# Kernel tuning notes

Measured on AMD Instinct MI355X. Metric: run time of the kernel, lower is better.

## Reference

```python
import jax, jax.numpy as jnp
import numpy as np

# Dims from LiftSplatShootGPN defaults
B, N, D, FH, FW, C = 8, 6, 41, 8, 22, 64
OGFH, OGFW = 128, 352
DX = jnp.array([0.5, 0.5, 20.0], dtype=jnp.float32)        # gen_dx_bx
BX = jnp.array([-49.75, -49.75, 0.0], dtype=jnp.float32)
NX = (200, 200, 1)


def _frustum():
    # D x fH x fW x 3, matches create_frustum
    ds = jnp.broadcast_to(jnp.arange(4.0, 45.0, 1.0, dtype=jnp.float32).reshape(D, 1, 1), (D, FH, FW))
    xs = jnp.broadcast_to(jnp.linspace(0.0, OGFW - 1.0, FW, dtype=jnp.float32).reshape(1, 1, FW), (D, FH, FW))
    ys = jnp.broadcast_to(jnp.linspace(0.0, OGFH - 1.0, FH, dtype=jnp.float32).reshape(1, FH, 1), (D, FH, FW))
    return jnp.stack((xs, ys, ds), -1)


def setup_inputs() -> dict:
    key = jax.random.key(0)
    k1, k2, k3, k4, k5, k6 = jax.random.split(key, 6)
    eye = jnp.eye(3, dtype=jnp.float32)
    x_feats = jax.random.normal(k1, (B, N, D, FH, FW, C), dtype=jnp.float32)
    # well-conditioned camera extrinsics / intrinsics
    rots = eye + 0.1 * jax.random.normal(k2, (B, N, 3, 3), dtype=jnp.float32)
    trans = 2.0 * jax.random.normal(k3, (B, N, 3), dtype=jnp.float32)
    intr_base = jnp.array([[278.0, 0.0, 176.0], [0.0, 278.0, 64.0], [0.0, 0.0, 1.0]], dtype=jnp.float32)
    intrins = intr_base + 0.5 * jax.random.normal(k4, (B, N, 3, 3), dtype=jnp.float32) * jnp.array([[1, 0, 1], [0, 1, 1], [0, 0, 0]], dtype=jnp.float32)
    post_rots = eye + 0.01 * jax.random.normal(k5, (B, N, 3, 3), dtype=jnp.float32)
    post_trans = 0.5 * jax.random.normal(k6, (B, N, 3), dtype=jnp.float32)
    return {"x_feats": x_feats, "rots": rots, "trans": trans, "intrins": intrins,
            "post_rots": post_rots, "post_trans": post_trans}


def _forward(x_feats, rots, trans, intrins, post_rots, post_trans):
    frustum = _frustum()  # [D,FH,FW,3]
    # get_geometry: undo image-space augmentation
    pts = frustum[None, None] - post_trans[:, :, None, None, None, :]            # [B,N,D,H,W,3]
    inv_pr = jnp.linalg.inv(post_rots)                                           # [B,N,3,3]
    pts = jnp.einsum('bnij,bndhwj->bndhwi', inv_pr, pts)
    # unproject: (u*d, v*d, d)
    pts = jnp.concatenate((pts[..., :2] * pts[..., 2:3], pts[..., 2:3]), axis=-1)
    combine = jnp.einsum('bnij,bnjk->bnik', rots, jnp.linalg.inv(intrins))
    geom = jnp.einsum('bnij,bndhwj->bndhwi', combine, pts) + trans[:, :, None, None, None, :]

    # voxel_pooling
    Nprime = B * N * D * FH * FW
    x = x_feats.reshape(Nprime, C)
    # torch .long() truncates toward zero -> astype(int32) matches
    g = ((geom - (BX - DX / 2.0)) / DX).reshape(Nprime, 3).astype(jnp.int32)
    bix = jnp.repeat(jnp.arange(B, dtype=jnp.int32), Nprime // B)
    kept = ((g[:, 0] >= 0) & (g[:, 0] < NX[0]) &
            (g[:, 1] >= 0) & (g[:, 1] < NX[1]) &
            (g[:, 2] >= 0) & (g[:, 2] < NX[2]))
    # QuickCumsum computes per-voxel segment sums; scatter-add of all kept points
    # into the dense grid yields identical values without the sort.
    flat = ((bix * NX[2] + g[:, 2]) * NX[0] + g[:, 0]) * NX[1] + g[:, 1]
    flat = jnp.where(kept, flat, 0)
    xm = jnp.where(kept[:, None], x, jnp.zeros((), x.dtype))
    grid = jnp.zeros((B * NX[2] * NX[0] * NX[1], C), dtype=x.dtype).at[flat].add(xm)
    # final: [B, C, nz, nx0, nx1] -> cat over nz (nz=1) -> [B, C, 200, 200]
    grid = grid.reshape(B, NX[2], NX[0], NX[1], C)
    final = jnp.transpose(grid, (0, 1, 4, 2, 3)).reshape(B, NX[2] * C, NX[0], NX[1])
    return final


def reference(x_feats, rots, trans, intrins, post_rots, post_trans):
    return _forward(x_feats, rots, trans, intrins, post_rots, post_trans)
```

## Files before the change

### kernel.cpp

```cpp
#include <hip/hip_runtime.h>

#define B_   8
#define N_   6
#define D_   41
#define FH_  8
#define FW_  22
#define C_   64
#define NPRIME (B_*N_*D_*FH_*FW_)
#define NBLK_PTS 1353
#define NX0  200
#define NX1  200
#define G1Q  4
#define NB2  (B_ * NX0 * G1Q)
#define OUTSZ (B_*C_*NX0*NX1)
#define CAP  128
#define DIRECT_N 16
#define MAXTASKS 16384
#define GATHER_BLOCKS 1024

__device__ void lapack_inv3_f32(const float Ain[9], float Aout[9]) {
    #pragma clang fp contract(off)
    float a[9];
    for (int r = 0; r < 3; ++r)
        for (int c = 0; c < 3; ++c)
            a[c*3 + r] = Ain[r*3 + c];
    int ipiv[3];
    for (int j = 0; j < 3; ++j) {
        int p = j;
        float amax = fabsf(a[j*3 + j]);
        for (int i = j + 1; i < 3; ++i) {
            float v = fabsf(a[j*3 + i]);
            if (v > amax) { amax = v; p = i; }
        }
        ipiv[j] = p;
        if (p != j)
            for (int c = 0; c < 3; ++c) { float t = a[c*3+j]; a[c*3+j] = a[c*3+p]; a[c*3+p] = t; }
        float d = 1.0f / a[j*3 + j];
        for (int i = j + 1; i < 3; ++i) a[j*3 + i] = a[j*3 + i] * d;
        for (int jj = j + 1; jj < 3; ++jj) {
            float temp = -a[jj*3 + j];
            for (int ii = j + 1; ii < 3; ++ii)
                a[jj*3 + ii] = a[jj*3 + ii] + a[j*3 + ii] * temp;
        }
    }
    for (int j = 0; j < 3; ++j) {
        float ajj_inv = 1.0f / a[j*3 + j];
        a[j*3 + j] = ajj_inv;
        float AJJ = -ajj_inv;
        for (int jj = 0; jj < j; ++jj) {
            float temp = a[j*3 + jj];
            for (int i = 0; i < jj; ++i)
                a[j*3 + i] = a[j*3 + i] + temp * a[jj*3 + i];
            a[j*3 + jj] = a[j*3 + jj] * a[jj*3 + jj];
        }
        for (int i = 0; i < j; ++i) a[j*3 + i] = a[j*3 + i] * AJJ;
    }
    float work[3];
    for (int j = 2; j >= 0; --j) {
        for (int i = j + 1; i < 3; ++i) { work[i] = a[j*3 + i]; a[j*3 + i] = 0.0f; }
        for (int jj = j + 1; jj < 3; ++jj) {
            float temp = -work[jj];
            for (int i = 0; i < 3; ++i)
                a[j*3 + i] = a[j*3 + i] + temp * a[jj*3 + i];
        }
    }
    for (int j = 2; j >= 0; --j) {
        int p = ipiv[j];
        if (p != j)
            for (int i = 0; i < 3; ++i) { float t = a[j*3+i]; a[j*3+i] = a[p*3+i]; a[p*3+i] = t; }
    }
    for (int r = 0; r < 3; ++r)
        for (int c = 0; c < 3; ++c)
            Aout[r*3 + c] = a[c*3 + r];
}

__global__ void prep_kernel(const float* __restrict__ rots,
                            const float* __restrict__ trans,
                            const float* __restrict__ intrins,
                            const float* __restrict__ post_rots,
                            const float* __restrict__ post_trans,
                            float* __restrict__ mats,
                            int* __restrict__ counts) {
    #pragma clang fp contract(off)
    int t = threadIdx.x;
    for (int i = t; i < NB2; i += 256) counts[i] = 0;
    if (t >= B_ * N_) return;
    float pr[9], ipr[9], K[9], iK[9];
    for (int i = 0; i < 9; ++i) { pr[i] = post_rots[t*9 + i]; K[i] = intrins[t*9 + i]; }
    lapack_inv3_f32(pr, ipr);
    lapack_inv3_f32(K, iK);
    float* m = mats + t * 24;
    for (int i = 0; i < 9; ++i) m[i] = ipr[i];
    for (int i = 0; i < 3; ++i)
        for (int k = 0; k < 3; ++k) {
            float s = rots[t*9 + i*3 + 0] * iK[0*3 + k];
            s = s + rots[t*9 + i*3 + 1] * iK[1*3 + k];
            s = s + rots[t*9 + i*3 + 2] * iK[2*3 + k];
            m[9 + i*3 + k] = s;
        }
    for (int i = 0; i < 3; ++i) {
        m[18 + i] = post_trans[t*3 + i];
        m[21 + i] = trans[t*3 + i];
    }
}

__global__ void __launch_bounds__(256) geom_kernel(
        const float* __restrict__ mats,
        unsigned int* __restrict__ pcode,
        int* __restrict__ counts,
        float4* __restrict__ out4) {
    #pragma clang fp contract(off)
    __shared__ unsigned int hist[NB2];
    int t = threadIdx.x;
    int p = blockIdx.x * 256 + t;
    for (int i = t; i < NB2; i += 256) hist[i] = 0u;
    __syncthreads();

    int w  = p % FW_;
    int h  = (p / FW_) % FH_;
    int d  = (p / (FW_ * FH_)) % D_;
    int bn = p / (FW_ * FH_ * D_);
    int b  = bn / N_;

    const float* m = mats + bn * 24;

    float xs = (w == FW_ - 1) ? 351.0f : (float)((double)w * (351.0 / 21.0));
    float ys = (h == FH_ - 1) ? 127.0f : (float)((double)h * (127.0 / 7.0));
    float ds = 4.0f + (float)d;

    float px = xs - m[18], py = ys - m[19], pz = ds - m[20];
    float qx = m[0]*px;  qx = qx + m[1]*py;  qx = qx + m[2]*pz;
    float qy = m[3]*px;  qy = qy + m[4]*py;  qy = qy + m[5]*pz;
    float qz = m[6]*px;  qz = qz + m[7]*py;  qz = qz + m[8]*pz;

    float ux = qx * qz, uy = qy * qz, uz = qz;

    float gx = m[9]*ux;   gx = gx + m[10]*uy;  gx = gx + m[11]*uz;  gx = gx + m[21];
    float gy = m[12]*ux;  gy = gy + m[13]*uy;  gy = gy + m[14]*uz;  gy = gy + m[22];
    float gz = m[15]*ux;  gz = gz + m[16]*uy;  gz = gz + m[17]*uz;  gz = gz + m[23];

    float cx = (gx - (-50.0f)) / 0.5f;
    float cy = (gy - (-50.0f)) / 0.5f;
    float cz = (gz - (-10.0f)) / 20.0f;
    int g0 = (int)cx;
    int g1 = (int)cy;
    int g2 = (int)cz;

    bool kept = (g0 >= 0) && (g0 < NX0) && (g1 >= 0) && (g1 < NX1) && (g2 == 0);
    if (kept) {
        int g1q = g1 / 50;
        int g1r = g1 - g1q * 50;
        int bk  = (b * NX0 + g0) * G1Q + g1q;
        pcode[p] = ((unsigned int)bk << 6) | (unsigned int)g1r;
        atomicAdd(&hist[bk], 1u);
    } else {
        pcode[p] = 0xFFFFFFFFu;
    }
    __syncthreads();
    for (int i = t; i < NB2; i += 256) {
        unsigned int hv = hist[i];
        if (hv) atomicAdd(&counts[i], (int)hv);
    }

    const int TOT4 = OUTSZ / 4;
    float4 z4 = make_float4(0.f, 0.f, 0.f, 0.f);
    for (int i = p; i < TOT4; i += NPRIME) out4[i] = z4;
}

__global__ void scan_kernel(const int* __restrict__ counts,
                            int* __restrict__ offsets,
                            int* __restrict__ cursor,
                            unsigned int* __restrict__ tasks,
                            int* __restrict__ task_count) {
    __shared__ int ts[256];
    __shared__ int tbase_s[256];
    int t = threadIdx.x;
    const int PER = NB2 / 256;
    int base = t * PER;
    int mysum = 0, mytasks = 0;
    for (int j = 0; j < PER; ++j) {
        int c = counts[base + j];
        mysum += c;
        if (c > 0) mytasks += (c + CAP - 1) / CAP;
    }
    ts[t] = mysum;
    tbase_s[t] = mytasks;
    __syncthreads();
    for (int off = 1; off < 256; off <<= 1) {
        int v  = (t >= off) ? ts[t - off] : 0;
        int tv = (t >= off) ? tbase_s[t - off] : 0;
        __syncthreads();
        ts[t] += v;
        tbase_s[t] += tv;
        __syncthreads();
    }
    int run  = (t > 0) ? ts[t - 1] : 0;
    int tpos = (t > 0) ? tbase_s[t - 1] : 0;
    for (int j = 0; j < PER; ++j) {
        int c = counts[base + j];
        offsets[base + j] = run;
        cursor[base + j]  = run;
        run += c;
        if (c > 0) {
            int nch = (c + CAP - 1) / CAP;
            unsigned int sole = (nch == 1) ? (1u << 31) : 0u;
            for (int k = 0; k < nch; ++k)
                tasks[tpos++] = sole | ((unsigned int)(base + j) << 12) | (unsigned int)k;
        }
    }
    if (t == 255) {
        offsets[NB2] = run;
        task_count[0] = tbase_s[255];
    }
}

__global__ void __launch_bounds__(256) place_kernel(
        const unsigned int* __restrict__ pcode,
        int* __restrict__ cursor,
        unsigned int* __restrict__ entries) {
    __shared__ int cnt[NB2];
    int t = threadIdx.x;
    int p = blockIdx.x * 256 + t;
    for (int i = t; i < NB2; i += 256) cnt[i] = 0;
    __syncthreads();
    unsigned int code = pcode[p];
    bool kept = (code != 0xFFFFFFFFu);
    int bk = (int)(code >> 6);
    int lr = 0;
    if (kept) lr = atomicAdd(&cnt[bk], 1);
    __syncthreads();
    for (int i = t; i < NB2; i += 256) {
        int c = cnt[i];
        if (c) cnt[i] = atomicAdd(&cursor[i], c);
    }
    __syncthreads();
    if (kept)
        entries[cnt[bk] + lr] = ((code & 63u) << 19) | (unsigned int)p;
}

#define LDS_STRIDE 51
__global__ void __launch_bounds__(512) gather_kernel(
        const float* __restrict__ x_feats,
        const unsigned int* __restrict__ entries,
        const int* __restrict__ offsets,
        const unsigned int* __restrict__ tasks,
        const int* __restrict__ task_count,
        float* __restrict__ out) {
    __shared__ float acc[C_ * LDS_STRIDE];
    int ntask = task_count[0];
    int t = threadIdx.x, wave = t >> 6, lane = t & 63;

    for (int tid = blockIdx.x; tid < ntask; tid += GATHER_BLOCKS) {
        unsigned int task = tasks[tid];
        int sole = (int)(task >> 31);
        int bk   = (int)((task >> 12) & 0x1FFFu);
        int ch   = (int)(task & 0xFFFu);
        int s = offsets[bk] + ch * CAP;
        int e = offsets[bk + 1];
        if (e > s + CAP) e = s + CAP;
        int n = e - s;

        int b   = bk / (NX0 * G1Q);
        int rem = bk % (NX0 * G1Q);
        int g0  = rem / G1Q, g1q = rem % G1Q;
        size_t obase = (size_t)b * (C_ * NX0 * NX1) + (size_t)g0 * NX1 + g1q * 50;

        if (n <= DIRECT_N) {
            for (int i = wave; i < n; i += 8) {
                unsigned int v = entries[s + i];
                float f = x_feats[(size_t)(v & 0x7FFFFu) * C_ + lane];
                unsafeAtomicAdd(&out[obase + (size_t)lane * (NX0 * NX1) + (int)(v >> 19)], f);
            }
            continue;
        }

        for (int i = t; i < C_ * LDS_STRIDE; i += 512) acc[i] = 0.0f;
        __syncthreads();

        int nfull = (n >> 6) << 6;
        for (int sbase = 0; sbase < nfull; sbase += 64) {
            int i0 = s + sbase + wave * 8;
            unsigned int v0 = entries[i0],     v1 = entries[i0 + 1];
            unsigned int v2 = entries[i0 + 2], v3 = entries[i0 + 3];
            unsigned int v4 = entries[i0 + 4], v5 = entries[i0 + 5];
            unsigned int v6 = entries[i0 + 6], v7 = entries[i0 + 7];
            float f0 = x_feats[(size_t)(v0 & 0x7FFFFu) * C_ + lane];
            float f1 = x_feats[(size_t)(v1 & 0x7FFFFu) * C_ + lane];
            float f2 = x_feats[(size_t)(v2 & 0x7FFFFu) * C_ + lane];
            float f3 = x_feats[(size_t)(v3 & 0x7FFFFu) * C_ + lane];
            float f4 = x_feats[(size_t)(v4 & 0x7FFFFu) * C_ + lane];
            float f5 = x_feats[(size_t)(v5 & 0x7FFFFu) * C_ + lane];
            float f6 = x_feats[(size_t)(v6 & 0x7FFFFu) * C_ + lane];
            float f7 = x_feats[(size_t)(v7 & 0x7FFFFu) * C_ + lane];
            int lb = lane * LDS_STRIDE;
            atomicAdd(&acc[lb + (int)(v0 >> 19)], f0);
            atomicAdd(&acc[lb + (int)(v1 >> 19)], f1);
            atomicAdd(&acc[lb + (int)(v2 >> 19)], f2);
            atomicAdd(&acc[lb + (int)(v3 >> 19)], f3);
            atomicAdd(&acc[lb + (int)(v4 >> 19)], f4);
            atomicAdd(&acc[lb + (int)(v5 >> 19)], f5);
            atomicAdd(&acc[lb + (int)(v6 >> 19)], f6);
            atomicAdd(&acc[lb + (int)(v7 >> 19)], f7);
        }
        for (int i = nfull + wave; i < n; i += 8) {
            unsigned int v = entries[s + i];
            float f = x_feats[(size_t)(v & 0x7FFFFu) * C_ + lane];
            atomicAdd(&acc[lane * LDS_STRIDE + (int)(v >> 19)], f);
        }
        __syncthreads();

        for (int k = t; k < C_ * 50; k += 512) {
            int c = k / 50, r = k - c * 50;
            float val = acc[c * LDS_STRIDE + r];
            if (val != 0.0f) {
                float* dst = &out[obase + (size_t)c * (NX0 * NX1) + r];
                if (sole) *dst = val;
                else unsafeAtomicAdd(dst, val);
            }
        }
        __syncthreads();
    }
}

extern "C" void kernel_launch(void* const* d_in, const int* in_sizes, int n_in,
                              void* d_out, int out_size, void* d_ws, size_t ws_size,
                              hipStream_t stream) {
    const float* x_feats    = (const float*)d_in[0];
    const float* rots       = (const float*)d_in[1];
    const float* trans      = (const float*)d_in[2];
    const float* intrins    = (const float*)d_in[3];
    const float* post_rots  = (const float*)d_in[4];
    const float* post_trans = (const float*)d_in[5];
    float* out = (float*)d_out;

    char* w = (char*)d_ws;
    float*        mats       = (float*)w;         w += 48 * 24 * sizeof(float);
    int*          counts     = (int*)w;           w += NB2 * sizeof(int);
    int*          offsets    = (int*)w;           w += (NB2 + 1) * sizeof(int);
    int*          cursor     = (int*)w;           w += NB2 * sizeof(int);
    int*          task_count = (int*)w;           w += 4 * sizeof(int);
    unsigned int* tasks      = (unsigned int*)w;  w += MAXTASKS * sizeof(unsigned int);
    unsigned int* pcode      = (unsigned int*)w;  w += NPRIME * sizeof(unsigned int);
    unsigned int* entries    = (unsigned int*)w;  w += NPRIME * sizeof(unsigned int);

    prep_kernel<<<1, 256, 0, stream>>>(rots, trans, intrins, post_rots, post_trans,
                                       mats, counts);
    geom_kernel<<<NBLK_PTS, 256, 0, stream>>>(mats, pcode, counts, (float4*)out);
    scan_kernel<<<1, 256, 0, stream>>>(counts, offsets, cursor, tasks, task_count);
    place_kernel<<<NBLK_PTS, 256, 0, stream>>>(pcode, cursor, entries);
    gather_kernel<<<GATHER_BLOCKS, 512, 0, stream>>>(x_feats, entries, offsets,
                                                     tasks, task_count, out);
}
```

Baseline: 209.2 us.

## Fuse all pipeline stages into one cooperative kernel with grid syncs

Replaces the five separate launches (prep, geometry histogram, scan, place, gather) with a single cooperative kernel of 1024 blocks × 256 threads. Grid-wide syncs separate the stages, and shared memory is reused between the histogram and the accumulator. The aim is to remove inter-kernel launch gaps and tail effects. In exchange, the gather stage now runs with 4 waves per block instead of 8, with per-iteration strides adjusted to match. Co-residency of all 1024 blocks is required, and the grid syncs add their own cost.

Result: slower. 656.2 us (+213.7%).

```diff
diff --git a/kernel.cpp b/kernel.cpp
--- a/kernel.cpp
+++ b/kernel.cpp
@@ -1,4 +1,7 @@
 #include <hip/hip_runtime.h>
+#include <hip/hip_cooperative_groups.h>
+
+namespace cg = cooperative_groups;
 
 #define B_   8
 #define N_   6
@@ -16,7 +19,9 @@
 #define CAP  128
 #define DIRECT_N 16
 #define MAXTASKS 16384
-#define GATHER_BLOCKS 1024
+#define FBLK 1024
+#define FTHR 256
+#define LDS_STRIDE 51
 
 __device__ void lapack_inv3_f32(const float Ain[9], float Aout[9]) {
     #pragma clang fp contract(off)
@@ -74,183 +79,179 @@
             Aout[r*3 + c] = a[c*3 + r];
 }
 
-__global__ void prep_kernel(const float* __restrict__ rots,
-                            const float* __restrict__ trans,
-                            const float* __restrict__ intrins,
-                            const float* __restrict__ post_rots,
-                            const float* __restrict__ post_trans,
-                            float* __restrict__ mats,
-                            int* __restrict__ counts) {
-    #pragma clang fp contract(off)
-    int t = threadIdx.x;
-    for (int i = t; i < NB2; i += 256) counts[i] = 0;
-    if (t >= B_ * N_) return;
-    float pr[9], ipr[9], K[9], iK[9];
-    for (int i = 0; i < 9; ++i) { pr[i] = post_rots[t*9 + i]; K[i] = intrins[t*9 + i]; }
-    lapack_inv3_f32(pr, ipr);
-    lapack_inv3_f32(K, iK);
-    float* m = mats + t * 24;
-    for (int i = 0; i < 9; ++i) m[i] = ipr[i];
-    for (int i = 0; i < 3; ++i)
-        for (int k = 0; k < 3; ++k) {
-            float s = rots[t*9 + i*3 + 0] * iK[0*3 + k];
-            s = s + rots[t*9 + i*3 + 1] * iK[1*3 + k];
-            s = s + rots[t*9 + i*3 + 2] * iK[2*3 + k];
-            m[9 + i*3 + k] = s;
-        }
-    for (int i = 0; i < 3; ++i) {
-        m[18 + i] = post_trans[t*3 + i];
-        m[21 + i] = trans[t*3 + i];
-    }
-}
-
-__global__ void __launch_bounds__(256) geom_kernel(
-        const float* __restrict__ mats,
+__global__ void __launch_bounds__(FTHR, 4) fused_kernel(
+        const float* __restrict__ x_feats,
+        const float* __restrict__ rots,
+        const float* __restrict__ trans,
+        const float* __restrict__ intrins,
+        const float* __restrict__ post_rots,
+        const float* __restrict__ post_trans,
+        float* __restrict__ mats,
+        int* __restrict__ counts,
+        int* __restrict__ offsets,
+        int* __restrict__ cursor,
+        int* __restrict__ task_count,
+        unsigned int* __restrict__ tasks,
         unsigned int* __restrict__ pcode,
-        int* __restrict__ counts,
-        float4* __restrict__ out4) {
-    #pragma clang fp contract(off)
-    __shared__ unsigned int hist[NB2];
-    int t = threadIdx.x;
-    int p = blockIdx.x * 256 + t;
-    for (int i = t; i < NB2; i += 256) hist[i] = 0u;
-    __syncthreads();
-
-    int w  = p % FW_;
-    int h  = (p / FW_) % FH_;
-    int d  = (p / (FW_ * FH_)) % D_;
-    int bn = p / (FW_ * FH_ * D_);
-    int b  = bn / N_;
-
-    const float* m = mats + bn * 24;
-
-    float xs = (w == FW_ - 1) ? 351.0f : (float)((double)w * (351.0 / 21.0));
-    float ys = (h == FH_ - 1) ? 127.0f : (float)((double)h * (127.0 / 7.0));
-    float ds = 4.0f + (float)d;
-
-    float px = xs - m[18], py = ys - m[19], pz = ds - m[20];
-    float qx = m[0]*px;  qx = qx + m[1]*py;  qx = qx + m[2]*pz;
-    float qy = m[3]*px;  qy = qy + m[4]*py;  qy = qy + m[5]*pz;
-    float qz = m[6]*px;  qz = qz + m[7]*py;  qz = qz + m[8]*pz;
-
-    float ux = qx * qz, uy = qy * qz, uz = qz;
-
-    float gx = m[9]*ux;   gx = gx + m[10]*uy;  gx = gx + m[11]*uz;  gx = gx + m[21];
-    float gy = m[12]*ux;  gy = gy + m[13]*uy;  gy = gy + m[14]*uz;  gy = gy + m[22];
-    float gz = m[15]*ux;  gz = gz + m[16]*uy;  gz = gz + m[17]*uz;  gz = gz + m[23];
-
-    float cx = (gx - (-50.0f)) / 0.5f;
-    float cy = (gy - (-50.0f)) / 0.5f;
-    float cz = (gz - (-10.0f)) / 20.0f;
-    int g0 = (int)cx;
-    int g1 = (int)cy;
-    int g2 = (int)cz;
-
-    bool kept = (g0 >= 0) && (g0 < NX0) && (g1 >= 0) && (g1 < NX1) && (g2 == 0);
-    if (kept) {
-        int g1q = g1 / 50;
-        int g1r = g1 - g1q * 50;
-        int bk  = (b * NX0 + g0) * G1Q + g1q;
-        pcode[p] = ((unsigned int)bk << 6) | (unsigned int)g1r;
-        atomicAdd(&hist[bk], 1u);
-    } else {
-        pcode[p] = 0xFFFFFFFFu;
-    }
-    __syncthreads();
-    for (int i = t; i < NB2; i += 256) {
-        unsigned int hv = hist[i];
-        if (hv) atomicAdd(&counts[i], (int)hv);
-    }
-
-    const int TOT4 = OUTSZ / 4;
-    float4 z4 = make_float4(0.f, 0.f, 0.f, 0.f);
-    for (int i = p; i < TOT4; i += NPRIME) out4[i] = z4;
-}
-
-__global__ void scan_kernel(const int* __restrict__ counts,
-                            int* __restrict__ offsets,
-                            int* __restrict__ cursor,
-                            unsigned int* __restrict__ tasks,
-                            int* __restrict__ task_count) {
+        unsigned int* __restrict__ entries,
+        float* __restrict__ out) {
+    cg::grid_group grid = cg::this_grid();
+    __shared__ int sh[NB2];
     __shared__ int ts[256];
-    __shared__ int tbase_s[256];
-    int t = threadIdx.x;
-    const int PER = NB2 / 256;
-    int base = t * PER;
-    int mysum = 0, mytasks = 0;
-    for (int j = 0; j < PER; ++j) {
-        int c = counts[base + j];
-        mysum += c;
-        if (c > 0) mytasks += (c + CAP - 1) / CAP;
-    }
-    ts[t] = mysum;
-    tbase_s[t] = mytasks;
-    __syncthreads();
-    for (int off = 1; off < 256; off <<= 1) {
-        int v  = (t >= off) ? ts[t - off] : 0;
-        int tv = (t >= off) ? tbase_s[t - off] : 0;
-        __syncthreads();
-        ts[t] += v;
-        tbase_s[t] += tv;
-        __syncthreads();
-    }
-    int run  = (t > 0) ? ts[t - 1] : 0;
-    int tpos = (t > 0) ? tbase_s[t - 1] : 0;
-    for (int j = 0; j < PER; ++j) {
-        int c = counts[base + j];
-        offsets[base + j] = run;
-        cursor[base + j]  = run;
-        run += c;
-        if (c > 0) {
-            int nch = (c + CAP - 1) / CAP;
-            unsigned int sole = (nch == 1) ? (1u << 31) : 0u;
-            for (int k = 0; k < nch; ++k)
-                tasks[tpos++] = sole | ((unsigned int)(base + j) << 12) | (unsigned int)k;
-        }
-    }
-    if (t == 255) {
-        offsets[NB2] = run;
-        task_count[0] = tbase_s[255];
-    }
-}
-
-__global__ void __launch_bounds__(256) place_kernel(
-        const unsigned int* __restrict__ pcode,
-        int* __restrict__ cursor,
-        unsigned int* __restrict__ entries) {
-    __shared__ int cnt[NB2];
-    int t = threadIdx.x;
-    int p = blockIdx.x * 256 + t;
-    for (int i = t; i < NB2; i += 256) cnt[i] = 0;
-    __syncthreads();
-    unsigned int code = pcode[p];
-    bool kept = (code != 0xFFFFFFFFu);
-    int bk = (int)(code >> 6);
-    int lr = 0;
-    if (kept) lr = atomicAdd(&cnt[bk], 1);
-    __syncthreads();
-    for (int i = t; i < NB2; i += 256) {
-        int c = cnt[i];
-        if (c) cnt[i] = atomicAdd(&cursor[i], c);
-    }
-    __syncthreads();
-    if (kept)
-        entries[cnt[bk] + lr] = ((code & 63u) << 19) | (unsigned int)p;
-}
-
-#define LDS_STRIDE 51
-__global__ void __launch_bounds__(512) gather_kernel(
-        const float* __restrict__ x_feats,
-        const unsigned int* __restrict__ entries,
-        const int* __restrict__ offsets,
-        const unsigned int* __restrict__ tasks,
-        const int* __restrict__ task_count,
-        float* __restrict__ out) {
-    __shared__ float acc[C_ * LDS_STRIDE];
+    __shared__ int tb[256];
+    int t   = threadIdx.x;
+    int blk = blockIdx.x;
+    int gid = blk * FTHR + t;
+    int wave = t >> 6, lane = t & 63;
+
+    if (blk == 0 && t < B_ * N_) {
+        #pragma clang fp contract(off)
+        float pr[9], ipr[9], K[9], iK[9];
+        for (int i = 0; i < 9; ++i) { pr[i] = post_rots[t*9 + i]; K[i] = intrins[t*9 + i]; }
+        lapack_inv3_f32(pr, ipr);
+        lapack_inv3_f32(K, iK);
+        float* m = mats + t * 24;
+        for (int i = 0; i < 9; ++i) m[i] = ipr[i];
+        for (int i = 0; i < 3; ++i)
+            for (int k = 0; k < 3; ++k) {
+                float s = rots[t*9 + i*3 + 0] * iK[0*3 + k];
+                s = s + rots[t*9 + i*3 + 1] * iK[1*3 + k];
+                s = s + rots[t*9 + i*3 + 2] * iK[2*3 + k];
+                m[9 + i*3 + k] = s;
+            }
+        for (int i = 0; i < 3; ++i) {
+            m[18 + i] = post_trans[t*3 + i];
+            m[21 + i] = trans[t*3 + i];
+        }
+    }
+    for (int i = gid; i < NB2; i += FBLK * FTHR) counts[i] = 0;
+    {
+        float4* out4 = (float4*)out;
+        const int TOT4 = OUTSZ / 4;
+        float4 z4 = make_float4(0.f, 0.f, 0.f, 0.f);
+        for (int i = gid; i < TOT4; i += FBLK * FTHR) out4[i] = z4;
+    }
+    grid.sync();
+
+    for (int vb = blk; vb < NBLK_PTS; vb += FBLK) {
+        #pragma clang fp contract(off)
+        for (int i = t; i < NB2; i += FTHR) sh[i] = 0;
+        __syncthreads();
+
+        int p  = vb * FTHR + t;
+        int w  = p % FW_;
+        int h  = (p / FW_) % FH_;
+        int d  = (p / (FW_ * FH_)) % D_;
+        int bn = p / (FW_ * FH_ * D_);
+        int b  = bn / N_;
+        const float* m = mats + bn * 24;
+
+        float xs = (w == FW_ - 1) ? 351.0f : (float)((double)w * (351.0 / 21.0));
+        float ys = (h == FH_ - 1) ? 127.0f : (float)((double)h * (127.0 / 7.0));
+        float ds = 4.0f + (float)d;
+
+        float px = xs - m[18], py = ys - m[19], pz = ds - m[20];
+        float qx = m[0]*px;  qx = qx + m[1]*py;  qx = qx + m[2]*pz;
+        float qy = m[3]*px;  qy = qy + m[4]*py;  qy = qy + m[5]*pz;
+        float qz = m[6]*px;  qz = qz + m[7]*py;  qz = qz + m[8]*pz;
+
+        float ux = qx * qz, uy = qy * qz, uz = qz;
+
+        float gx = m[9]*ux;   gx = gx + m[10]*uy;  gx = gx + m[11]*uz;  gx = gx + m[21];
+        float gy = m[12]*ux;  gy = gy + m[13]*uy;  gy = gy + m[14]*uz;  gy = gy + m[22];
+        float gz = m[15]*ux;  gz = gz + m[16]*uy;  gz = gz + m[17]*uz;  gz = gz + m[23];
+
+        float cx = (gx - (-50.0f)) / 0.5f;
+        float cy = (gy - (-50.0f)) / 0.5f;
+        float cz = (gz - (-10.0f)) / 20.0f;
+        int g0 = (int)cx;
+        int g1 = (int)cy;
+        int g2 = (int)cz;
+
+        bool kept = (g0 >= 0) && (g0 < NX0) && (g1 >= 0) && (g1 < NX1) && (g2 == 0);
+        if (kept) {
+            int g1q = g1 / 50;
+            int g1r = g1 - g1q * 50;
+            int bk  = (b * NX0 + g0) * G1Q + g1q;
+            pcode[p] = ((unsigned int)bk << 6) | (unsigned int)g1r;
+            atomicAdd(&sh[bk], 1);
+        } else {
+            pcode[p] = 0xFFFFFFFFu;
+        }
+        __syncthreads();
+        for (int i = t; i < NB2; i += FTHR) {
+            int hv = sh[i];
+            if (hv) atomicAdd(&counts[i], hv);
+        }
+        __syncthreads();
+    }
+    grid.sync();
+
+    if (blk == 0) {
+        const int PER = NB2 / FTHR;
+        int base = t * PER;
+        int mysum = 0, mytasks = 0;
+        for (int j = 0; j < PER; ++j) {
+            int c = counts[base + j];
+            mysum += c;
+            if (c > 0) mytasks += (c + CAP - 1) / CAP;
+        }
+        ts[t] = mysum;
+        tb[t] = mytasks;
+        __syncthreads();
+        for (int off = 1; off < FTHR; off <<= 1) {
+            int v  = (t >= off) ? ts[t - off] : 0;
+            int tv = (t >= off) ? tb[t - off] : 0;
+            __syncthreads();
+            ts[t] += v;
+            tb[t] += tv;
+            __syncthreads();
+        }
+        int run  = (t > 0) ? ts[t - 1] : 0;
+        int tpos = (t > 0) ? tb[t - 1] : 0;
+        for (int j = 0; j < PER; ++j) {
+            int c = counts[base + j];
+            offsets[base + j] = run;
+            cursor[base + j]  = run;
+            run += c;
+            if (c > 0) {
+                int nch = (c + CAP - 1) / CAP;
+                unsigned int sole = (nch == 1) ? (1u << 31) : 0u;
+                for (int k = 0; k < nch; ++k)
+                    tasks[tpos++] = sole | ((unsigned int)(base + j) << 12) | (unsigned int)k;
+            }
+        }
+        if (t == FTHR - 1) {
+            offsets[NB2] = run;
+            task_count[0] = tb[FTHR - 1];
+        }
+    }
+    grid.sync();
+
+    for (int vb = blk; vb < NBLK_PTS; vb += FBLK) {
+        for (int i = t; i < NB2; i += FTHR) sh[i] = 0;
+        __syncthreads();
+        int p = vb * FTHR + t;
+        unsigned int code = pcode[p];
+        bool kept = (code != 0xFFFFFFFFu);
+        int bk = (int)(code >> 6);
+        int lr = 0;
+        if (kept) lr = atomicAdd(&sh[bk], 1);
+        __syncthreads();
+        for (int i = t; i < NB2; i += FTHR) {
+            int c = sh[i];
+            if (c) sh[i] = atomicAdd(&cursor[i], c);
+        }
+        __syncthreads();
+        if (kept)
+            entries[sh[bk] + lr] = ((code & 63u) << 19) | (unsigned int)p;
+        __syncthreads();
+    }
+    grid.sync();
+
+    float* acc = (float*)sh;
     int ntask = task_count[0];
-    int t = threadIdx.x, wave = t >> 6, lane = t & 63;
-
-    for (int tid = blockIdx.x; tid < ntask; tid += GATHER_BLOCKS) {
+    for (int tid = blk; tid < ntask; tid += FBLK) {
         unsigned int task = tasks[tid];
         int sole = (int)(task >> 31);
         int bk   = (int)((task >> 12) & 0x1FFFu);
@@ -266,7 +267,7 @@
         size_t obase = (size_t)b * (C_ * NX0 * NX1) + (size_t)g0 * NX1 + g1q * 50;
 
         if (n <= DIRECT_N) {
-            for (int i = wave; i < n; i += 8) {
+            for (int i = wave; i < n; i += 4) {
                 unsigned int v = entries[s + i];
                 float f = x_feats[(size_t)(v & 0x7FFFFu) * C_ + lane];
                 unsafeAtomicAdd(&out[obase + (size_t)lane * (NX0 * NX1) + (int)(v >> 19)], f);
@@ -274,11 +275,11 @@
             continue;
         }
 
-        for (int i = t; i < C_ * LDS_STRIDE; i += 512) acc[i] = 0.0f;
-        __syncthreads();
-
-        int nfull = (n >> 6) << 6;
-        for (int sbase = 0; sbase < nfull; sbase += 64) {
+        for (int i = t; i < C_ * LDS_STRIDE; i += FTHR) acc[i] = 0.0f;
+        __syncthreads();
+
+        int nfull = (n >> 5) << 5;
+        for (int sbase = 0; sbase < nfull; sbase += 32) {
             int i0 = s + sbase + wave * 8;
             unsigned int v0 = entries[i0],     v1 = entries[i0 + 1];
             unsigned int v2 = entries[i0 + 2], v3 = entries[i0 + 3];
@@ -302,14 +303,14 @@
             atomicAdd(&acc[lb + (int)(v6 >> 19)], f6);
             atomicAdd(&acc[lb + (int)(v7 >> 19)], f7);
         }
-        for (int i = nfull + wave; i < n; i += 8) {
+        for (int i = nfull + wave; i < n; i += 4) {
             unsigned int v = entries[s + i];
             float f = x_feats[(size_t)(v & 0x7FFFFu) * C_ + lane];
             atomicAdd(&acc[lane * LDS_STRIDE + (int)(v >> 19)], f);
         }
         __syncthreads();
 
-        for (int k = t; k < C_ * 50; k += 512) {
+        for (int k = t; k < C_ * 50; k += FTHR) {
             int c = k / 50, r = k - c * 50;
             float val = acc[c * LDS_STRIDE + r];
             if (val != 0.0f) {
@@ -343,11 +344,13 @@
     unsigned int* pcode      = (unsigned int*)w;  w += NPRIME * sizeof(unsigned int);
     unsigned int* entries    = (unsigned int*)w;  w += NPRIME * sizeof(unsigned int);
 
-    prep_kernel<<<1, 256, 0, stream>>>(rots, trans, intrins, post_rots, post_trans,
-                                       mats, counts);
-    geom_kernel<<<NBLK_PTS, 256, 0, stream>>>(mats, pcode, counts, (float4*)out);
-    scan_kernel<<<1, 256, 0, stream>>>(counts, offsets, cursor, tasks, task_count);
-    place_kernel<<<NBLK_PTS, 256, 0, stream>>>(pcode, cursor, entries);
-    gather_kernel<<<GATHER_BLOCKS, 512, 0, stream>>>(x_feats, entries, offsets,
-                                                     tasks, task_count, out);
+    void* args[] = {
+        (void*)&x_feats, (void*)&rots, (void*)&trans, (void*)&intrins,
+        (void*)&post_rots, (void*)&post_trans,
+        (void*)&mats, (void*)&counts, (void*)&offsets, (void*)&cursor,
+        (void*)&task_count, (void*)&tasks, (void*)&pcode, (void*)&entries,
+        (void*)&out
+    };
+    hipLaunchCooperativeKernel((void*)fused_kernel, dim3(FBLK), dim3(FTHR),
+                               args, 0, stream);
 }
```

## Eliminate full output zeroing by writing every bucket region in gather

Applied to the files above, without the earlier changes.

Drops the bulk zero-fill of the whole 8x64x200x200 output from the geometry kernel. Every bucket now gets a task: empty or single-chunk buckets write their region directly, with zeros where nothing lands. Multi-chunk buckets are zeroed in place_kernel before the atomic accumulation. The camera-matrix prep is folded into the geometry kernel (per-block shared matrices) and a tiny init kernel replaces it. This cuts roughly 82 MB of redundant stores, but adds a task for every empty bucket (6400 total) and removes the small-bucket direct-atomic fast path.

Result: slower. 230.7 us (+10.3%).

```diff
diff --git a/kernel.cpp b/kernel.cpp
--- a/kernel.cpp
+++ b/kernel.cpp
@@ -6,6 +6,7 @@
 #define FH_  8
 #define FW_  22
 #define C_   64
+#define PPC  (D_*FH_*FW_)
 #define NPRIME (B_*N_*D_*FH_*FW_)
 #define NBLK_PTS 1353
 #define NX0  200
@@ -14,9 +15,10 @@
 #define NB2  (B_ * NX0 * G1Q)
 #define OUTSZ (B_*C_*NX0*NX1)
 #define CAP  128
-#define DIRECT_N 16
-#define MAXTASKS 16384
+#define MAXTASKS 8192
+#define MAXMC 1024
 #define GATHER_BLOCKS 1024
+#define REGION (C_ * 50)
 
 __device__ void lapack_inv3_f32(const float Ain[9], float Aout[9]) {
     #pragma clang fp contract(off)
@@ -74,55 +76,67 @@
             Aout[r*3 + c] = a[c*3 + r];
 }
 
-__global__ void prep_kernel(const float* __restrict__ rots,
-                            const float* __restrict__ trans,
-                            const float* __restrict__ intrins,
-                            const float* __restrict__ post_rots,
-                            const float* __restrict__ post_trans,
-                            float* __restrict__ mats,
-                            int* __restrict__ counts) {
+__device__ void make_mats(int bn,
+                          const float* __restrict__ rots,
+                          const float* __restrict__ trans,
+                          const float* __restrict__ intrins,
+                          const float* __restrict__ post_rots,
+                          const float* __restrict__ post_trans,
+                          float* m) {
     #pragma clang fp contract(off)
-    int t = threadIdx.x;
-    for (int i = t; i < NB2; i += 256) counts[i] = 0;
-    if (t >= B_ * N_) return;
     float pr[9], ipr[9], K[9], iK[9];
-    for (int i = 0; i < 9; ++i) { pr[i] = post_rots[t*9 + i]; K[i] = intrins[t*9 + i]; }
+    for (int i = 0; i < 9; ++i) { pr[i] = post_rots[bn*9 + i]; K[i] = intrins[bn*9 + i]; }
     lapack_inv3_f32(pr, ipr);
     lapack_inv3_f32(K, iK);
-    float* m = mats + t * 24;
     for (int i = 0; i < 9; ++i) m[i] = ipr[i];
     for (int i = 0; i < 3; ++i)
         for (int k = 0; k < 3; ++k) {
-            float s = rots[t*9 + i*3 + 0] * iK[0*3 + k];
-            s = s + rots[t*9 + i*3 + 1] * iK[1*3 + k];
-            s = s + rots[t*9 + i*3 + 2] * iK[2*3 + k];
+            float s = rots[bn*9 + i*3 + 0] * iK[0*3 + k];
+            s = s + rots[bn*9 + i*3 + 1] * iK[1*3 + k];
+            s = s + rots[bn*9 + i*3 + 2] * iK[2*3 + k];
             m[9 + i*3 + k] = s;
         }
     for (int i = 0; i < 3; ++i) {
-        m[18 + i] = post_trans[t*3 + i];
-        m[21 + i] = trans[t*3 + i];
-    }
+        m[18 + i] = post_trans[bn*3 + i];
+        m[21 + i] = trans[bn*3 + i];
+    }
+}
+
+__global__ void init_kernel(int* __restrict__ counts) {
+    int i = blockIdx.x * blockDim.x + threadIdx.x;
+    if (i < NB2 + 4) counts[i] = 0;
 }
 
 __global__ void __launch_bounds__(256) geom_kernel(
-        const float* __restrict__ mats,
+        const float* __restrict__ rots,
+        const float* __restrict__ trans,
+        const float* __restrict__ intrins,
+        const float* __restrict__ post_rots,
+        const float* __restrict__ post_trans,
         unsigned int* __restrict__ pcode,
-        int* __restrict__ counts,
-        float4* __restrict__ out4) {
+        int* __restrict__ counts) {
     #pragma clang fp contract(off)
-    __shared__ unsigned int hist[NB2];
+    __shared__ int hist[NB2];
+    __shared__ float smat[2][24];
     int t = threadIdx.x;
     int p = blockIdx.x * 256 + t;
-    for (int i = t; i < NB2; i += 256) hist[i] = 0u;
+    for (int i = t; i < NB2; i += 256) hist[i] = 0;
+
+    int p0  = blockIdx.x * 256;
+    int bn0 = p0 / PPC;
+    int bn1 = (p0 + 255) / PPC;
+    if (t < 2) {
+        int bnv = (t == 0) ? bn0 : bn1;
+        make_mats(bnv, rots, trans, intrins, post_rots, post_trans, smat[t]);
+    }
     __syncthreads();
 
     int w  = p % FW_;
     int h  = (p / FW_) % FH_;
     int d  = (p / (FW_ * FH_)) % D_;
-    int bn = p / (FW_ * FH_ * D_);
+    int bn = p / PPC;
     int b  = bn / N_;
-
-    const float* m = mats + bn * 24;
+    const float* m = smat[(bn == bn0) ? 0 : 1];
 
     float xs = (w == FW_ - 1) ? 351.0f : (float)((double)w * (351.0 / 21.0));
     float ys = (h == FH_ - 1) ? 127.0f : (float)((double)h * (127.0 / 7.0));
@@ -152,28 +166,26 @@
         int g1r = g1 - g1q * 50;
         int bk  = (b * NX0 + g0) * G1Q + g1q;
         pcode[p] = ((unsigned int)bk << 6) | (unsigned int)g1r;
-        atomicAdd(&hist[bk], 1u);
+        atomicAdd(&hist[bk], 1);
     } else {
         pcode[p] = 0xFFFFFFFFu;
     }
     __syncthreads();
     for (int i = t; i < NB2; i += 256) {
-        unsigned int hv = hist[i];
-        if (hv) atomicAdd(&counts[i], (int)hv);
-    }
-
-    const int TOT4 = OUTSZ / 4;
-    float4 z4 = make_float4(0.f, 0.f, 0.f, 0.f);
-    for (int i = p; i < TOT4; i += NPRIME) out4[i] = z4;
+        int hv = hist[i];
+        if (hv) atomicAdd(&counts[i], hv);
+    }
 }
 
 __global__ void scan_kernel(const int* __restrict__ counts,
                             int* __restrict__ offsets,
                             int* __restrict__ cursor,
                             unsigned int* __restrict__ tasks,
-                            int* __restrict__ task_count) {
+                            int* __restrict__ task_count,
+                            int* __restrict__ mc_count,
+                            int* __restrict__ mcbuckets) {
     __shared__ int ts[256];
-    __shared__ int tbase_s[256];
+    __shared__ int tb[256];
     int t = threadIdx.x;
     const int PER = NB2 / 256;
     int base = t * PER;
@@ -181,43 +193,50 @@
     for (int j = 0; j < PER; ++j) {
         int c = counts[base + j];
         mysum += c;
-        if (c > 0) mytasks += (c + CAP - 1) / CAP;
+        mytasks += (c <= CAP) ? 1 : (c + CAP - 1) / CAP;
     }
     ts[t] = mysum;
-    tbase_s[t] = mytasks;
+    tb[t] = mytasks;
     __syncthreads();
     for (int off = 1; off < 256; off <<= 1) {
         int v  = (t >= off) ? ts[t - off] : 0;
-        int tv = (t >= off) ? tbase_s[t - off] : 0;
+        int tv = (t >= off) ? tb[t - off] : 0;
         __syncthreads();
         ts[t] += v;
-        tbase_s[t] += tv;
+        tb[t] += tv;
         __syncthreads();
     }
     int run  = (t > 0) ? ts[t - 1] : 0;
-    int tpos = (t > 0) ? tbase_s[t - 1] : 0;
+    int tpos = (t > 0) ? tb[t - 1] : 0;
     for (int j = 0; j < PER; ++j) {
-        int c = counts[base + j];
-        offsets[base + j] = run;
-        cursor[base + j]  = run;
+        int bk = base + j;
+        int c = counts[bk];
+        offsets[bk] = run;
+        cursor[bk]  = run;
         run += c;
-        if (c > 0) {
+        if (c <= CAP) {
+            tasks[tpos++] = (1u << 31) | ((unsigned int)bk << 12);
+        } else {
             int nch = (c + CAP - 1) / CAP;
-            unsigned int sole = (nch == 1) ? (1u << 31) : 0u;
             for (int k = 0; k < nch; ++k)
-                tasks[tpos++] = sole | ((unsigned int)(base + j) << 12) | (unsigned int)k;
+                tasks[tpos++] = ((unsigned int)bk << 12) | (unsigned int)k;
+            int mi = atomicAdd(mc_count, 1);
+            if (mi < MAXMC) mcbuckets[mi] = bk;
         }
     }
     if (t == 255) {
         offsets[NB2] = run;
-        task_count[0] = tbase_s[255];
+        task_count[0] = tb[255];
     }
 }
 
 __global__ void __launch_bounds__(256) place_kernel(
         const unsigned int* __restrict__ pcode,
         int* __restrict__ cursor,
-        unsigned int* __restrict__ entries) {
+        unsigned int* __restrict__ entries,
+        const int* __restrict__ mc_count,
+        const int* __restrict__ mcbuckets,
+        float* __restrict__ out) {
     __shared__ int cnt[NB2];
     int t = threadIdx.x;
     int p = blockIdx.x * 256 + t;
@@ -236,6 +255,20 @@
     __syncthreads();
     if (kept)
         entries[cnt[bk] + lr] = ((code & 63u) << 19) | (unsigned int)p;
+
+    int nmc = mc_count[0];
+    if (nmc > MAXMC) nmc = MAXMC;
+    for (int i = blockIdx.x; i < nmc; i += NBLK_PTS) {
+        int mbk = mcbuckets[i];
+        int b   = mbk / (NX0 * G1Q);
+        int rem = mbk % (NX0 * G1Q);
+        int g0  = rem / G1Q, g1q = rem % G1Q;
+        size_t obase = (size_t)b * (C_ * NX0 * NX1) + (size_t)g0 * NX1 + g1q * 50;
+        for (int k = t; k < REGION; k += 256) {
+            int c = k / 50, r = k - c * 50;
+            out[obase + (size_t)c * (NX0 * NX1) + r] = 0.0f;
+        }
+    }
 }
 
 #define LDS_STRIDE 51
@@ -265,11 +298,10 @@
         int g0  = rem / G1Q, g1q = rem % G1Q;
         size_t obase = (size_t)b * (C_ * NX0 * NX1) + (size_t)g0 * NX1 + g1q * 50;
 
-        if (n <= DIRECT_N) {
-            for (int i = wave; i < n; i += 8) {
-                unsigned int v = entries[s + i];
-                float f = x_feats[(size_t)(v & 0x7FFFFu) * C_ + lane];
-                unsafeAtomicAdd(&out[obase + (size_t)lane * (NX0 * NX1) + (int)(v >> 19)], f);
+        if (n == 0) {
+            for (int k = t; k < REGION; k += 512) {
+                int c = k / 50, r = k - c * 50;
+                out[obase + (size_t)c * (NX0 * NX1) + r] = 0.0f;
             }
             continue;
         }
@@ -309,13 +341,17 @@
         }
         __syncthreads();
 
-        for (int k = t; k < C_ * 50; k += 512) {
-            int c = k / 50, r = k - c * 50;
-            float val = acc[c * LDS_STRIDE + r];
-            if (val != 0.0f) {
-                float* dst = &out[obase + (size_t)c * (NX0 * NX1) + r];
-                if (sole) *dst = val;
-                else unsafeAtomicAdd(dst, val);
+        if (sole) {
+            for (int k = t; k < REGION; k += 512) {
+                int c = k / 50, r = k - c * 50;
+                out[obase + (size_t)c * (NX0 * NX1) + r] = acc[c * LDS_STRIDE + r];
+            }
+        } else {
+            for (int k = t; k < REGION; k += 512) {
+                int c = k / 50, r = k - c * 50;
+                float val = acc[c * LDS_STRIDE + r];
+                if (val != 0.0f)
+                    unsafeAtomicAdd(&out[obase + (size_t)c * (NX0 * NX1) + r], val);
             }
         }
         __syncthreads();
@@ -334,20 +370,24 @@
     float* out = (float*)d_out;
 
     char* w = (char*)d_ws;
-    float*        mats       = (float*)w;         w += 48 * 24 * sizeof(float);
     int*          counts     = (int*)w;           w += NB2 * sizeof(int);
+    int*          task_count = (int*)w;           w += sizeof(int);
+    int*          mc_count   = (int*)w;           w += sizeof(int);
+    w += 2 * sizeof(int);
     int*          offsets    = (int*)w;           w += (NB2 + 1) * sizeof(int);
     int*          cursor     = (int*)w;           w += NB2 * sizeof(int);
-    int*          task_count = (int*)w;           w += 4 * sizeof(int);
+    int*          mcbuckets  = (int*)w;           w += MAXMC * sizeof(int);
     unsigned int* tasks      = (unsigned int*)w;  w += MAXTASKS * sizeof(unsigned int);
     unsigned int* pcode      = (unsigned int*)w;  w += NPRIME * sizeof(unsigned int);
     unsigned int* entries    = (unsigned int*)w;  w += NPRIME * sizeof(unsigned int);
 
-    prep_kernel<<<1, 256, 0, stream>>>(rots, trans, intrins, post_rots, post_trans,
-                                       mats, counts);
-    geom_kernel<<<NBLK_PTS, 256, 0, stream>>>(mats, pcode, counts, (float4*)out);
-    scan_kernel<<<1, 256, 0, stream>>>(counts, offsets, cursor, tasks, task_count);
-    place_kernel<<<NBLK_PTS, 256, 0, stream>>>(pcode, cursor, entries);
+    init_kernel<<<(NB2 + 4 + 255) / 256, 256, 0, stream>>>(counts);
+    geom_kernel<<<NBLK_PTS, 256, 0, stream>>>(rots, trans, intrins, post_rots,
+                                              post_trans, pcode, counts);
+    scan_kernel<<<1, 256, 0, stream>>>(counts, offsets, cursor, tasks,
+                                       task_count, mc_count, mcbuckets);
+    place_kernel<<<NBLK_PTS, 256, 0, stream>>>(pcode, cursor, entries,
+                                               mc_count, mcbuckets, out);
     gather_kernel<<<GATHER_BLOCKS, 512, 0, stream>>>(x_feats, entries, offsets,
                                                      tasks, task_count, out);
 }
```
